# Optimization experiments

Hardware: AMD Instinct MI355X
Metric: run time of the kernel (lower is better)

Reference implementation:

```python
import jax, jax.numpy as jnp
import numpy as np

NEG_INF_SCALE = -1e9


def setup_inputs() -> dict:
    key = jax.random.key(0)
    ks = jax.random.split(key, 8)
    B, T, M, D = 64, 1024, 256, 1024
    query = jax.random.normal(ks[0], (B, 1, M), dtype=jnp.float32)
    keys = jax.random.normal(ks[1], (B, T, M), dtype=jnp.float32)
    values = jax.random.normal(ks[2], (B, T, D), dtype=jnp.float32)
    mask = jax.random.randint(ks[3], (B, 1, T), 0, 2).astype(jnp.float32)
    # MLP params (scaled like torch default init ~ 1/sqrt(fan_in))
    W1 = jax.random.normal(ks[4], (4 * M, D), dtype=jnp.float32) / np.sqrt(4 * M)
    b1 = jnp.zeros((D,), dtype=jnp.float32)
    W2 = jax.random.normal(ks[5], (D, D), dtype=jnp.float32) / np.sqrt(D)
    b2 = jnp.zeros((D,), dtype=jnp.float32)
    w_score = jax.random.normal(ks[6], (D, 1), dtype=jnp.float32) / np.sqrt(D)
    b_score = jnp.zeros((1,), dtype=jnp.float32)
    return {"query": query, "keys": keys, "values": values, "mask": mask,
            "W1": W1, "b1": b1, "W2": W2, "b2": b2,
            "w_score": w_score, "b_score": b_score}


def reference(query, keys, values, mask, W1, b1, W2, b2, w_score, b_score):
    # query: [B,1,M] broadcast against keys: [B,T,M]
    q = jnp.broadcast_to(query, keys.shape)
    att_input = jnp.concatenate([q, keys, q - keys, q * keys], axis=-1)  # [B,T,4M]
    h = jax.nn.relu(att_input @ W1 + b1)   # [B,T,D]
    h = jax.nn.relu(h @ W2 + b2)           # [B,T,D]
    score = h @ w_score + b_score          # [B,T,1]
    logits = jnp.swapaxes(score, 1, 2)     # [B,1,T]
    logits = logits + mask * NEG_INF_SCALE
    attn = jax.nn.softmax(logits, axis=-1)  # [B,1,T]
    out = jnp.matmul(attn, values)          # [B,1,D]
    return out
```

## Files before the change

### kernel.cpp

```cpp
#include <hip/hip_runtime.h>

#define DEV __device__ __forceinline__

typedef __attribute__((ext_vector_type(4))) float f32x4;
typedef __attribute__((ext_vector_type(8))) short short8;
typedef __attribute__((ext_vector_type(4))) short s16x4;
typedef __attribute__((ext_vector_type(4))) float f32x4v;

DEV short f2bf(float f) {
  union { float f; unsigned u; } v; v.f = f;
  unsigned r = (v.u + 0x7FFFu + ((v.u >> 16) & 1u)) >> 16;
  return (short)r;
}

DEV void gload16(const void* g, void* l) {
  __builtin_amdgcn_global_load_lds(
      (const __attribute__((address_space(1))) void*)g,
      (__attribute__((address_space(3))) void*)l, 16, 0, 0);
}

#define BAR() __builtin_amdgcn_s_barrier()
#define LGKMW(n)                                              \
  {                                                           \
    asm volatile("s_waitcnt lgkmcnt(" #n ")" ::: "memory");   \
    __builtin_amdgcn_sched_barrier(0);                        \
  }
#define VMW(n)                                                \
  {                                                           \
    asm volatile("s_waitcnt vmcnt(" #n ")" ::: "memory");     \
    __builtin_amdgcn_sched_barrier(0);                        \
  }


__global__ __launch_bounds__(256) void k_prep_keys(const float* __restrict__ k,
                                                   short* __restrict__ o) {
  int i = (blockIdx.x * 256 + threadIdx.x) * 8;
  f32x4v v0 = *(const f32x4v*)(k + i);
  f32x4v v1 = *(const f32x4v*)(k + i + 4);
  short8 s;
  s[0] = f2bf(v0[0]); s[1] = f2bf(v0[1]); s[2] = f2bf(v0[2]); s[3] = f2bf(v0[3]);
  s[4] = f2bf(v1[0]); s[5] = f2bf(v1[1]); s[6] = f2bf(v1[2]); s[7] = f2bf(v1[3]);
  *(short8*)(o + i) = s;
}

__global__ __launch_bounds__(256) void k_prep_w2f(const float* __restrict__ w2,
                                                  short* __restrict__ w2f) {
  __shared__ float tile[64][65];
  const int kt = blockIdx.x, n0 = blockIdx.y * 64;
  const int a = threadIdx.x & 63, q = threadIdx.x >> 6;
#pragma unroll
  for (int i = 0; i < 16; ++i) {
    int kk = i * 4 + q;
    tile[kk][a] = w2[(size_t)(kt * 64 + kk) * 1024 + n0 + a];
  }
  __syncthreads();
  const int l = threadIdx.x & 63, cgl = threadIdx.x >> 6;
#pragma unroll
  for (int kh = 0; kh < 2; ++kh) {
    short8 v;
#pragma unroll
    for (int j = 0; j < 8; ++j)
      v[j] = f2bf(tile[kh * 32 + (l >> 4) * 8 + j][cgl * 16 + (l & 15)]);
    *(short8*)&w2f[((size_t)((kt * 2 + kh) * 64 + (n0 >> 4) + cgl)) * 512 + l * 8] = v;
  }
}

__global__ __launch_bounds__(256) void k_prep_wkt4(const float* __restrict__ w1,
                                                   const float* __restrict__ query,
                                                   const float* __restrict__ b1,
                                                   short* __restrict__ wktf,
                                                   float* __restrict__ biasb) {
  __shared__ short tile[4][64][72];
  __shared__ float qlds[4][256];
  __shared__ float redm[4][64][4];
  const int bg = blockIdx.x, d0g = blockIdx.y, d0 = d0g * 64;
  const int tid = threadIdx.x;
  const int d = tid & 63, mq = tid >> 6;

  for (int idx = tid; idx < 1024; idx += 256)
    qlds[idx >> 8][idx & 255] = query[(bg * 4 + (idx >> 8)) * 256 + (idx & 255)];
  __syncthreads();

  float bacc[4] = {0.f, 0.f, 0.f, 0.f};
  const int l = tid & 63, cgl = tid >> 6;

  for (int mc = 0; mc < 4; ++mc) {
#pragma unroll 4
    for (int i = 0; i < 16; ++i) {
      int ml = i * 4 + mq;
      int m = mc * 64 + ml;
      float wa = w1[(size_t)m * 1024 + d0 + d];
      float wb = w1[(size_t)(256 + m) * 1024 + d0 + d];
      float wc = w1[(size_t)(512 + m) * 1024 + d0 + d];
      float wd = w1[(size_t)(768 + m) * 1024 + d0 + d];
      float bc = wb - wc, ac = wa + wc;
#pragma unroll
      for (int bb = 0; bb < 4; ++bb) {
        float qv = qlds[bb][m];
        tile[bb][d][ml] = f2bf(bc + qv * wd);
        bacc[bb] += qv * ac;
      }
    }
    __syncthreads();
#pragma unroll
    for (int bb = 0; bb < 4; ++bb) {
      short* ob = wktf + (size_t)(bg * 4 + bb) * 262144;
#pragma unroll
      for (int kh = 0; kh < 2; ++kh) {
        short8 v = *(const short8*)&tile[bb][cgl * 16 + (l & 15)]
                                        [kh * 32 + (l >> 4) * 8];
        *(short8*)&ob[((size_t)((mc * 2 + kh) * 64 + d0g * 4 + cgl)) * 512 + l * 8] = v;
      }
    }
    __syncthreads();
  }

  redm[0][d][mq] = bacc[0];
  redm[1][d][mq] = bacc[1];
  redm[2][d][mq] = bacc[2];
  redm[3][d][mq] = bacc[3];
  __syncthreads();
  const int bb = tid >> 6, dd = tid & 63;
  biasb[(bg * 4 + bb) * 1024 + d0 + dd] =
      redm[bb][dd][0] + redm[bb][dd][1] + redm[bb][dd][2] + redm[bb][dd][3] +
      b1[d0 + dd];
}


template <int MODE>
__global__ __launch_bounds__(256, 2) void k_gemm(const short* __restrict__ A,
                                                 const short* __restrict__ Bf,
                                                 const float* __restrict__ bias,
                                                 const float* __restrict__ wscore,
                                                 short* __restrict__ hout,
                                                 float* __restrict__ spart) {
  __shared__ short lds[32768];
  constexpr int SK = (MODE == 1) ? 256 : 1024;
  constexpr int KT = (MODE == 1) ? 4 : 16;

  const int tid = threadIdx.x;
  const int bx = blockIdx.x;
  const int L = (bx & 7) * 256 + (bx >> 3);

  const short *Ab, *Bb;
  const float *biasp, *wsp = nullptr;
  short* houtp = nullptr;
  int rt, ct;
  if constexpr (MODE == 1) {
    const int b = L >> 5;
    rt = (L >> 2) & 7; ct = L & 3;
    Ab = A + ((size_t)(b * 1024 + rt * 128)) * 256;
    Bb = Bf + (size_t)b * 262144;
    biasp = bias + b * 1024 + ct * 256;
    houtp = hout + ((size_t)(b * 1024 + rt * 128)) * 1024 + ct * 256;
  } else {
    rt = L >> 2; ct = L & 3;
    Ab = A + (size_t)rt * 128 * 1024;
    Bb = Bf;
    biasp = bias + ct * 256;
    wsp = wscore + ct * 256;
  }

  int gA[4], dA[4];
#pragma unroll
  for (int j = 0; j < 4; ++j) {
    int s = tid + j * 256, row = s >> 3, kc = (s & 7) ^ (row & 7);
    gA[j] = row * SK + kc * 8;
    dA[j] = s * 8;
  }
  auto STAGE = [&](int kt) {
    const int bb = (kt & 3) * 8192;
#pragma unroll
    for (int j = 0; j < 4; ++j) gload16(Ab + gA[j] + kt * 64, &lds[bb + dA[j]]);
  };

  const int lane = tid & 63, l15 = lane & 15, l4 = lane >> 4, wc = tid >> 6;
  const int afo0 = l15 * 64 + ((l4 ^ (l15 & 7)) * 8);
  const int afo1 = l15 * 64 + (((4 + l4) ^ (l15 & 7)) * 8);

  f32x4 acc[8][4];
#pragma unroll
  for (int m = 0; m < 8; ++m)
#pragma unroll
    for (int n = 0; n < 4; ++n) acc[m][n] = f32x4{0.f, 0.f, 0.f, 0.f};
  short8 bf[2][4][2];
  short8 af[8];

#define LOADB(kt, BK_)                                                          \
  _Pragma("unroll") for (int n_ = 0; n_ < 4; ++n_) {                            \
    _Pragma("unroll") for (int kh_ = 0; kh_ < 2; ++kh_) {                       \
      bf[BK_][n_][kh_] = *(const short8*)(Bb +                                  \
          ((size_t)(((kt) * 2 + kh_) * 64 + ct * 16 + n_ * 4 + wc) << 9) +      \
          lane * 8);                                                            \
    }                                                                           \
  }

  STAGE(0); LOADB(0, 0);
  STAGE(1); LOADB(1, 1);
  VMW(12);
  BAR();

#pragma unroll
  for (int t = 0; t < KT; ++t) {
    const int bb = (t & 3) * 8192;
#pragma unroll
    for (int m = 0; m < 8; ++m) af[m] = *(const short8*)&lds[bb + afo0 + m * 1024];
    LGKMW(0);
    __builtin_amdgcn_s_setprio(1);
#pragma unroll
    for (int m = 0; m < 8; ++m)
#pragma unroll
      for (int n = 0; n < 4; ++n)
        acc[m][n] = __builtin_amdgcn_mfma_f32_16x16x32_bf16(bf[t & 1][n][0], af[m],
                                                            acc[m][n], 0, 0, 0);
    __builtin_amdgcn_s_setprio(0);
#pragma unroll
    for (int m = 0; m < 8; ++m) af[m] = *(const short8*)&lds[bb + afo1 + m * 1024];
    if (t + 2 < KT) STAGE(t + 2);
    LGKMW(0);
    __builtin_amdgcn_s_setprio(1);
#pragma unroll
    for (int m = 0; m < 8; ++m)
#pragma unroll
      for (int n = 0; n < 4; ++n)
        acc[m][n] = __builtin_amdgcn_mfma_f32_16x16x32_bf16(bf[t & 1][n][1], af[m],
                                                            acc[m][n], 0, 0, 0);
    __builtin_amdgcn_s_setprio(0);
    if (t + 2 < KT) {
      LOADB(t + 2, (t & 1));
      VMW(12);
    } else {
      VMW(0);
    }
    BAR();
  }
#undef LOADB

  if constexpr (MODE == 1) {
    float bv[4][4];
#pragma unroll
    for (int n = 0; n < 4; ++n)
#pragma unroll
      for (int r2 = 0; r2 < 4; ++r2)
        bv[n][r2] = biasp[n * 64 + wc * 16 + l4 * 4 + r2];
#pragma unroll
    for (int m = 0; m < 8; ++m) {
      int row = m * 16 + l15;
#pragma unroll
      for (int n = 0; n < 4; ++n) {
        s16x4 pk;
#pragma unroll
        for (int r2 = 0; r2 < 4; ++r2)
          pk[r2] = f2bf(fmaxf(acc[m][n][r2] + bv[n][r2], 0.f));
        *(s16x4*)&houtp[(size_t)row * 1024 + n * 64 + wc * 16 + l4 * 4] = pk;
      }
    }
  } else {
    float bv[4][4], wv[4][4];
#pragma unroll
    for (int n = 0; n < 4; ++n)
#pragma unroll
      for (int r2 = 0; r2 < 4; ++r2) {
        int c = n * 64 + wc * 16 + l4 * 4 + r2;
        bv[n][r2] = biasp[c];
        wv[n][r2] = wsp[c];
      }
    float* so = spart + ((size_t)(ct * 4 + wc) << 16) + rt * 128;
#pragma unroll
    for (int m = 0; m < 8; ++m) {
      float s = 0.f;
#pragma unroll
      for (int n = 0; n < 4; ++n)
#pragma unroll
        for (int r2 = 0; r2 < 4; ++r2)
          s += fmaxf(acc[m][n][r2] + bv[n][r2], 0.f) * wv[n][r2];
      s += __shfl_xor(s, 16);
      s += __shfl_xor(s, 32);
      if (lane < 16) so[m * 16 + l15] = s;
    }
  }
}


__global__ __launch_bounds__(256) void k_softmax(const float* __restrict__ spart,
                                                 const float* __restrict__ mask,
                                                 const float* __restrict__ bscore,
                                                 float* __restrict__ attn) {
  const int b = blockIdx.x, tid = threadIdx.x;
  __shared__ float sm[1024];
  __shared__ float red[8];
  const float bs = bscore[0];
  float lmax = -3.0e38f;
  for (int t = tid; t < 1024; t += 256) {
    float s = bs;
#pragma unroll
    for (int c = 0; c < 16; ++c) s += spart[(size_t)c * 65536 + b * 1024 + t];
    float lg = s + mask[b * 1024 + t] * (-1e9f);
    sm[t] = lg;
    lmax = fmaxf(lmax, lg);
  }
  for (int o = 32; o; o >>= 1) lmax = fmaxf(lmax, __shfl_xor(lmax, o));
  const int wid = tid >> 6, lane = tid & 63;
  if (lane == 0) red[wid] = lmax;
  __syncthreads();
  float bmax = fmaxf(fmaxf(red[0], red[1]), fmaxf(red[2], red[3]));
  float lsum = 0.f;
  for (int t = tid; t < 1024; t += 256) {
    float e = __expf(sm[t] - bmax);
    sm[t] = e;
    lsum += e;
  }
  for (int o = 32; o; o >>= 1) lsum += __shfl_xor(lsum, o);
  __syncthreads();
  if (lane == 0) red[wid] = lsum;
  __syncthreads();
  float inv = 1.0f / (red[0] + red[1] + red[2] + red[3]);
  for (int t = tid; t < 1024; t += 256) attn[b * 1024 + t] = sm[t] * inv;
}

__global__ __launch_bounds__(256) void k_out(const float* __restrict__ attn,
                                             const float* __restrict__ values,
                                             float* __restrict__ part) {
  const int b = blockIdx.x >> 3, ts = blockIdx.x & 7;
  const int tid = threadIdx.x;
  __shared__ float at[128];
  if (tid < 128) at[tid] = attn[b * 1024 + ts * 128 + tid];
  __syncthreads();
  const float* vb = values + ((size_t)b * 1024 + ts * 128) * 1024 + tid * 4;
  f32x4 acc = {0.f, 0.f, 0.f, 0.f};
#pragma unroll 8
  for (int t = 0; t < 128; ++t) {
    f32x4v v = *(const f32x4v*)(vb + (size_t)t * 1024);
    float a = at[t];
    acc[0] += a * v[0]; acc[1] += a * v[1]; acc[2] += a * v[2]; acc[3] += a * v[3];
  }
  *(f32x4*)(part + ((size_t)(b * 8 + ts)) * 1024 + tid * 4) = acc;
}

__global__ __launch_bounds__(256) void k_red(const float* __restrict__ part,
                                             float* __restrict__ out) {
  const int b = blockIdx.x;
  const int c4 = threadIdx.x * 4;
  f32x4 s = {0.f, 0.f, 0.f, 0.f};
#pragma unroll
  for (int ts = 0; ts < 8; ++ts) {
    f32x4v v = *(const f32x4v*)(part + ((size_t)(b * 8 + ts)) * 1024 + c4);
    s[0] += v[0]; s[1] += v[1]; s[2] += v[2]; s[3] += v[3];
  }
  *(f32x4*)(out + b * 1024 + c4) = s;
}


extern "C" void kernel_launch(void* const* d_in, const int* in_sizes, int n_in,
                              void* d_out, int out_size, void* d_ws, size_t ws_size,
                              hipStream_t stream) {
  const float* query  = (const float*)d_in[0];
  const float* keys   = (const float*)d_in[1];
  const float* values = (const float*)d_in[2];
  const float* mask   = (const float*)d_in[3];
  const float* W1     = (const float*)d_in[4];
  const float* b1     = (const float*)d_in[5];
  const float* W2     = (const float*)d_in[6];
  const float* b2     = (const float*)d_in[7];
  const float* wscore = (const float*)d_in[8];
  const float* bscore = (const float*)d_in[9];
  float* out = (float*)d_out;

  char* ws = (char*)d_ws;
  short* keysb = (short*)(ws);
  short* wktf  = (short*)(ws + 33554432ull);
  short* w2f   = (short*)(ws + 67108864ull);
  float* biasb = (float*)(ws + 69206016ull);
  short* h1    = (short*)(ws + 69468160ull);
  float* spart = (float*)(ws + 203685888ull);
  float* attn  = (float*)(ws + 207880192ull);
  float* part  = (float*)(ws + 208142336ull);

  k_prep_keys<<<8192, 256, 0, stream>>>(keys, keysb);
  k_prep_w2f<<<dim3(16, 16), 256, 0, stream>>>(W2, w2f);
  k_prep_wkt4<<<dim3(16, 16), 256, 0, stream>>>(W1, query, b1, wktf, biasb);

  k_gemm<1><<<2048, 256, 0, stream>>>(keysb, wktf, biasb, nullptr, h1, nullptr);
  k_gemm<2><<<2048, 256, 0, stream>>>(h1, w2f, b2, wscore, nullptr, spart);

  k_softmax<<<64, 256, 0, stream>>>(spart, mask, bscore, attn);
  k_out<<<512, 256, 0, stream>>>(attn, values, part);
  k_red<<<64, 256, 0, stream>>>(part, out);
}
```

Baseline: 268.8 us.

## Switch GEMM inner loop to 32x32x16 bf16 MFMA with matching weight layout

```diff
diff --git a/kernel.cpp b/kernel.cpp
--- a/kernel.cpp
+++ b/kernel.cpp
@@ -3,6 +3,7 @@
 #define DEV __device__ __forceinline__
 
 typedef __attribute__((ext_vector_type(4))) float f32x4;
+typedef __attribute__((ext_vector_type(16))) float f32x16;
 typedef __attribute__((ext_vector_type(8))) short short8;
 typedef __attribute__((ext_vector_type(4))) short s16x4;
 typedef __attribute__((ext_vector_type(4))) float f32x4v;
@@ -54,14 +55,14 @@
     tile[kk][a] = w2[(size_t)(kt * 64 + kk) * 1024 + n0 + a];
   }
   __syncthreads();
-  const int l = threadIdx.x & 63, cgl = threadIdx.x >> 6;
-#pragma unroll
-  for (int kh = 0; kh < 2; ++kh) {
+  const int l = threadIdx.x & 63, kcl = threadIdx.x >> 6;
+#pragma unroll
+  for (int cbl = 0; cbl < 2; ++cbl) {
     short8 v;
 #pragma unroll
     for (int j = 0; j < 8; ++j)
-      v[j] = f2bf(tile[kh * 32 + (l >> 4) * 8 + j][cgl * 16 + (l & 15)]);
-    *(short8*)&w2f[((size_t)((kt * 2 + kh) * 64 + (n0 >> 4) + cgl)) * 512 + l * 8] = v;
+      v[j] = f2bf(tile[kcl * 16 + (l >> 5) * 8 + j][cbl * 32 + (l & 31)]);
+    *(short8*)&w2f[((size_t)((kt * 4 + kcl) * 32 + (n0 >> 5) + cbl)) * 512 + l * 8] = v;
   }
 }
 
@@ -82,7 +83,7 @@
   __syncthreads();
 
   float bacc[4] = {0.f, 0.f, 0.f, 0.f};
-  const int l = tid & 63, cgl = tid >> 6;
+  const int l = tid & 63, kcl = tid >> 6;
 
   for (int mc = 0; mc < 4; ++mc) {
 #pragma unroll 4
@@ -106,10 +107,10 @@
     for (int bb = 0; bb < 4; ++bb) {
       short* ob = wktf + (size_t)(bg * 4 + bb) * 262144;
 #pragma unroll
-      for (int kh = 0; kh < 2; ++kh) {
-        short8 v = *(const short8*)&tile[bb][cgl * 16 + (l & 15)]
-                                        [kh * 32 + (l >> 4) * 8];
-        *(short8*)&ob[((size_t)((mc * 2 + kh) * 64 + d0g * 4 + cgl)) * 512 + l * 8] = v;
+      for (int cbl = 0; cbl < 2; ++cbl) {
+        short8 v = *(const short8*)&tile[bb][cbl * 32 + (l & 31)]
+                                        [kcl * 16 + (l >> 5) * 8];
+        *(short8*)&ob[((size_t)((mc * 4 + kcl) * 32 + d0g * 2 + cbl)) * 512 + l * 8] = v;
       }
     }
     __syncthreads();
@@ -174,23 +175,27 @@
     for (int j = 0; j < 4; ++j) gload16(Ab + gA[j] + kt * 64, &lds[bb + dA[j]]);
   };
 
-  const int lane = tid & 63, l15 = lane & 15, l4 = lane >> 4, wc = tid >> 6;
-  const int afo0 = l15 * 64 + ((l4 ^ (l15 & 7)) * 8);
-  const int afo1 = l15 * 64 + (((4 + l4) ^ (l15 & 7)) * 8);
-
-  f32x4 acc[8][4];
-#pragma unroll
-  for (int m = 0; m < 8; ++m)
-#pragma unroll
-    for (int n = 0; n < 4; ++n) acc[m][n] = f32x4{0.f, 0.f, 0.f, 0.f};
-  short8 bf[2][4][2];
-  short8 af[8];
+  const int lane = tid & 63, l31 = lane & 31, l5 = lane >> 5, wc = tid >> 6;
+  int afo[4];
+#pragma unroll
+  for (int kk = 0; kk < 4; ++kk)
+    afo[kk] = l31 * 64 + (((kk * 2 + l5) ^ (lane & 7)) * 8);
+
+  f32x16 acc[4][2];
+#pragma unroll
+  for (int m = 0; m < 4; ++m)
+#pragma unroll
+    for (int n = 0; n < 2; ++n)
+#pragma unroll
+      for (int r = 0; r < 16; ++r) acc[m][n][r] = 0.f;
+  short8 bf[2][2][4];
+  short8 af[4][2];
 
 #define LOADB(kt, BK_)                                                          \
-  _Pragma("unroll") for (int n_ = 0; n_ < 4; ++n_) {                            \
-    _Pragma("unroll") for (int kh_ = 0; kh_ < 2; ++kh_) {                       \
-      bf[BK_][n_][kh_] = *(const short8*)(Bb +                                  \
-          ((size_t)(((kt) * 2 + kh_) * 64 + ct * 16 + n_ * 4 + wc) << 9) +      \
+  _Pragma("unroll") for (int n_ = 0; n_ < 2; ++n_) {                            \
+    _Pragma("unroll") for (int kk_ = 0; kk_ < 4; ++kk_) {                       \
+      bf[BK_][n_][kk_] = *(const short8*)(Bb +                                  \
+          ((size_t)(((kt) * 4 + kk_) * 32 + ct * 8 + wc * 2 + n_) << 9) +       \
           lane * 8);                                                            \
     }                                                                           \
   }
@@ -204,27 +209,39 @@
   for (int t = 0; t < KT; ++t) {
     const int bb = (t & 3) * 8192;
 #pragma unroll
-    for (int m = 0; m < 8; ++m) af[m] = *(const short8*)&lds[bb + afo0 + m * 1024];
+    for (int m = 0; m < 4; ++m) {
+      af[m][0] = *(const short8*)&lds[bb + afo[0] + m * 2048];
+      af[m][1] = *(const short8*)&lds[bb + afo[1] + m * 2048];
+    }
     LGKMW(0);
     __builtin_amdgcn_s_setprio(1);
 #pragma unroll
-    for (int m = 0; m < 8; ++m)
-#pragma unroll
-      for (int n = 0; n < 4; ++n)
-        acc[m][n] = __builtin_amdgcn_mfma_f32_16x16x32_bf16(bf[t & 1][n][0], af[m],
-                                                            acc[m][n], 0, 0, 0);
+    for (int m = 0; m < 4; ++m)
+#pragma unroll
+      for (int n = 0; n < 2; ++n) {
+        acc[m][n] = __builtin_amdgcn_mfma_f32_32x32x16_bf16(bf[t & 1][n][0],
+                                                            af[m][0], acc[m][n], 0, 0, 0);
+        acc[m][n] = __builtin_amdgcn_mfma_f32_32x32x16_bf16(bf[t & 1][n][1],
+                                                            af[m][1], acc[m][n], 0, 0, 0);
+      }
     __builtin_amdgcn_s_setprio(0);
 #pragma unroll
-    for (int m = 0; m < 8; ++m) af[m] = *(const short8*)&lds[bb + afo1 + m * 1024];
+    for (int m = 0; m < 4; ++m) {
+      af[m][0] = *(const short8*)&lds[bb + afo[2] + m * 2048];
+      af[m][1] = *(const short8*)&lds[bb + afo[3] + m * 2048];
+    }
     if (t + 2 < KT) STAGE(t + 2);
     LGKMW(0);
     __builtin_amdgcn_s_setprio(1);
 #pragma unroll
-    for (int m = 0; m < 8; ++m)
-#pragma unroll
-      for (int n = 0; n < 4; ++n)
-        acc[m][n] = __builtin_amdgcn_mfma_f32_16x16x32_bf16(bf[t & 1][n][1], af[m],
-                                                            acc[m][n], 0, 0, 0);
+    for (int m = 0; m < 4; ++m)
+#pragma unroll
+      for (int n = 0; n < 2; ++n) {
+        acc[m][n] = __builtin_amdgcn_mfma_f32_32x32x16_bf16(bf[t & 1][n][2],
+                                                            af[m][0], acc[m][n], 0, 0, 0);
+        acc[m][n] = __builtin_amdgcn_mfma_f32_32x32x16_bf16(bf[t & 1][n][3],
+                                                            af[m][1], acc[m][n], 0, 0, 0);
+      }
     __builtin_amdgcn_s_setprio(0);
     if (t + 2 < KT) {
       LOADB(t + 2, (t & 1));
@@ -237,46 +254,53 @@
 #undef LOADB
 
   if constexpr (MODE == 1) {
-    float bv[4][4];
-#pragma unroll
-    for (int n = 0; n < 4; ++n)
-#pragma unroll
-      for (int r2 = 0; r2 < 4; ++r2)
-        bv[n][r2] = biasp[n * 64 + wc * 16 + l4 * 4 + r2];
-#pragma unroll
-    for (int m = 0; m < 8; ++m) {
-      int row = m * 16 + l15;
-#pragma unroll
-      for (int n = 0; n < 4; ++n) {
-        s16x4 pk;
+    float bv[2][4][4];
+#pragma unroll
+    for (int n = 0; n < 2; ++n)
+#pragma unroll
+      for (int q = 0; q < 4; ++q)
 #pragma unroll
         for (int r2 = 0; r2 < 4; ++r2)
-          pk[r2] = f2bf(fmaxf(acc[m][n][r2] + bv[n][r2], 0.f));
-        *(s16x4*)&houtp[(size_t)row * 1024 + n * 64 + wc * 16 + l4 * 4] = pk;
-      }
+          bv[n][q][r2] = biasp[wc * 64 + n * 32 + q * 8 + l5 * 4 + r2];
+#pragma unroll
+    for (int m = 0; m < 4; ++m) {
+      int row = m * 32 + l31;
+#pragma unroll
+      for (int n = 0; n < 2; ++n)
+#pragma unroll
+        for (int q = 0; q < 4; ++q) {
+          s16x4 pk;
+#pragma unroll
+          for (int r2 = 0; r2 < 4; ++r2)
+            pk[r2] = f2bf(fmaxf(acc[m][n][q * 4 + r2] + bv[n][q][r2], 0.f));
+          *(s16x4*)&houtp[(size_t)row * 1024 + wc * 64 + n * 32 + q * 8 + l5 * 4] = pk;
+        }
     }
   } else {
-    float bv[4][4], wv[4][4];
-#pragma unroll
-    for (int n = 0; n < 4; ++n)
-#pragma unroll
-      for (int r2 = 0; r2 < 4; ++r2) {
-        int c = n * 64 + wc * 16 + l4 * 4 + r2;
-        bv[n][r2] = biasp[c];
-        wv[n][r2] = wsp[c];
-      }
+    float bv[2][4][4], wv[2][4][4];
+#pragma unroll
+    for (int n = 0; n < 2; ++n)
+#pragma unroll
+      for (int q = 0; q < 4; ++q)
+#pragma unroll
+        for (int r2 = 0; r2 < 4; ++r2) {
+          int c = wc * 64 + n * 32 + q * 8 + l5 * 4 + r2;
+          bv[n][q][r2] = biasp[c];
+          wv[n][q][r2] = wsp[c];
+        }
     float* so = spart + ((size_t)(ct * 4 + wc) << 16) + rt * 128;
 #pragma unroll
-    for (int m = 0; m < 8; ++m) {
+    for (int m = 0; m < 4; ++m) {
       float s = 0.f;
 #pragma unroll
-      for (int n = 0; n < 4; ++n)
-#pragma unroll
-        for (int r2 = 0; r2 < 4; ++r2)
-          s += fmaxf(acc[m][n][r2] + bv[n][r2], 0.f) * wv[n][r2];
-      s += __shfl_xor(s, 16);
+      for (int n = 0; n < 2; ++n)
+#pragma unroll
+        for (int q = 0; q < 4; ++q)
+#pragma unroll
+          for (int r2 = 0; r2 < 4; ++r2)
+            s += fmaxf(acc[m][n][q * 4 + r2] + bv[n][q][r2], 0.f) * wv[n][q][r2];
       s += __shfl_xor(s, 32);
-      if (lane < 16) so[m * 16 + l15] = s;
+      if (lane < 32) so[m * 32 + l31] = s;
     }
   }
 }
```

Result: slower. 297.0 us (+10.5%).
